# Kernel optimization log

Measured on AMD Instinct MI355X. Metric: run time of the kernel, lower is better.

The kernel has to match this reference:

```python
import jax, jax.numpy as jnp
import numpy as np
from jax import lax

NUM_ITERS = 3
EPSILON = 0.5
QUEUE = 32768
NUM_CLUSTER = 1000


def setup_inputs() -> dict:
    key = jax.random.key(0)
    k1, _ = jax.random.split(key)
    memory_logits = jax.random.normal(k1, (QUEUE, NUM_CLUSTER), dtype=jnp.float32)
    learn_k = jnp.ones((1,), dtype=jnp.float32) * 5.0  # init value in torch module
    return {"memory_logits": memory_logits, "learn_k": learn_k}


def reference(memory_logits, learn_k):
    C = memory_logits.shape[1]
    # stabilize then exp, transpose to [C, N]
    ml = memory_logits - jnp.max(memory_logits)
    Q = jnp.exp(ml / EPSILON).T  # [C, N]
    # K: softmax over clusters of w * log(sigmoid(learn_k)); w = n/(C-1)
    w = (jnp.arange(C, dtype=Q.dtype) / (C - 1)).reshape(1, -1)
    K = jax.nn.softmax(w * jnp.log(jax.nn.sigmoid(learn_k)), axis=1)  # [1, C]
    Kcol = K.reshape(-1, 1)  # [C, 1] for row-wise scaling of Q
    B = Q.shape[1]
    # sort rows by descending row-sum
    order = jnp.argsort(-jnp.sum(Q, axis=1))
    Q = Q[order]
    Q = Q / jnp.sum(Q)

    def body(Q, _):
        Q = Q / jnp.sum(Q, axis=1, keepdims=True)   # row normalize
        Q = Q * Kcol                                 # (Q.t() * K).t()
        Q = jnp.clip(Q, 1e-16, None)
        Q = Q / jnp.sum(Q, axis=0, keepdims=True)   # col normalize
        Q = Q / B
        return Q, None

    Q, _ = lax.scan(body, Q, None, length=NUM_ITERS)
    Q = Q * B
    reorder = jnp.argsort(order)
    Q = Q[reorder]
    return Q.T  # [N, C]
```

## Files before the change

kernel.cpp:

```cpp
#include <hip/hip_runtime.h>
#include <math.h>

#define NQ 32768
#define NC 1000
#define NC4 250

__device__ __forceinline__ float wredsum(float v) {
#pragma unroll
    for (int off = 32; off > 0; off >>= 1) v += __shfl_xor(v, off, 64);
    return v;
}

__global__ __launch_bounds__(256) void k_colsum_exp(const float* __restrict__ in,
                                                    float* __restrict__ S) {
    __shared__ float sacc[NC];
    for (int i = threadIdx.x; i < NC; i += 256) sacc[i] = 0.f;
    __syncthreads();
    const int lane = threadIdx.x & 63;
    const int nw = (gridDim.x * 256) >> 6;
    const int wave = (blockIdx.x * 256 + threadIdx.x) >> 6;
    float acc[16];
#pragma unroll
    for (int i = 0; i < 16; ++i) acc[i] = 0.f;
    for (int row = wave; row < NQ; row += nw) {
        const float4* rp = reinterpret_cast<const float4*>(in + (size_t)row * NC);
#pragma unroll
        for (int k = 0; k < 4; ++k) {
            int c4 = k * 64 + lane;
            if (c4 < NC4) {
                float4 a = rp[c4];
                acc[4 * k + 0] += __expf(2.0f * a.x);
                acc[4 * k + 1] += __expf(2.0f * a.y);
                acc[4 * k + 2] += __expf(2.0f * a.z);
                acc[4 * k + 3] += __expf(2.0f * a.w);
            }
        }
    }
#pragma unroll
    for (int k = 0; k < 4; ++k) {
        int c4 = k * 64 + lane;
        if (c4 < NC4) {
            atomicAdd(&sacc[4 * c4 + 0], acc[4 * k + 0]);
            atomicAdd(&sacc[4 * c4 + 1], acc[4 * k + 1]);
            atomicAdd(&sacc[4 * c4 + 2], acc[4 * k + 2]);
            atomicAdd(&sacc[4 * c4 + 3], acc[4 * k + 3]);
        }
    }
    __syncthreads();
    for (int i = threadIdx.x; i < NC; i += 256) atomicAdd(&S[i], sacc[i]);
}

__global__ __launch_bounds__(1024) void k_rank(const float* __restrict__ S,
                                               const float* __restrict__ learn_k,
                                               float* __restrict__ Ksc,
                                               float* __restrict__ R) {
    __shared__ float sS[NC];
    __shared__ float sred[16];
    const int tid = threadIdx.x;
    for (int i = tid; i < NC; i += 1024) sS[i] = S[i];
    __syncthreads();
    const float L = -log1pf(expf(-learn_k[0]));
    float part = 0.f;
    for (int i = tid; i < NC; i += 1024)
        part += expf(((float)i * (1.0f / 999.0f)) * L);
    part = wredsum(part);
    if ((tid & 63) == 0) sred[tid >> 6] = part;
    __syncthreads();
    if (tid == 0) {
        float s = 0.f;
        for (int i = 0; i < 16; ++i) s += sred[i];
        sred[0] = s;
    }
    __syncthreads();
    const float denom = sred[0];
    for (int c = tid; c < NC; c += 1024) {
        float sc = sS[c];
        int p = 0;
        for (int j = 0; j < NC; ++j) {
            float sj = sS[j];
            p += (sj > sc) || (sj == sc && j < c);
        }
        float ks = expf(((float)p * (1.0f / 999.0f)) * L) / denom;
        Ksc[c] = ks;
        R[c] = ks / sc;
    }
}

__global__ __launch_bounds__(256) void k_prepR(const float* __restrict__ Ksc,
                                               const float* __restrict__ S,
                                               float* __restrict__ R) {
    int i = blockIdx.x * blockDim.x + threadIdx.x;
    if (i < NC) R[i] = Ksc[i] / S[i];
}

template <bool EXPIN, bool ACC>
__global__ __launch_bounds__(256) void k_iter(const float* __restrict__ in,
                                              float* __restrict__ out,
                                              const float* __restrict__ R,
                                              float* __restrict__ Snext) {
    __shared__ float sacc[NC];
    if (ACC) {
        for (int i = threadIdx.x; i < NC; i += 256) sacc[i] = 0.f;
        __syncthreads();
    }
    const int lane = threadIdx.x & 63;
    const int nw = (gridDim.x * 256) >> 6;
    const int wave = (blockIdx.x * 256 + threadIdx.x) >> 6;

    float4 rf[4];
    const float4* R4 = reinterpret_cast<const float4*>(R);
#pragma unroll
    for (int k = 0; k < 4; ++k) {
        int c4 = k * 64 + lane;
        rf[k] = (c4 < NC4) ? R4[c4] : make_float4(0.f, 0.f, 0.f, 0.f);
    }
    float acc[16];
#pragma unroll
    for (int i = 0; i < 16; ++i) acc[i] = 0.f;

    float4 nxt[4];
#pragma unroll
    for (int k = 0; k < 4; ++k) nxt[k] = make_float4(0.f, 0.f, 0.f, 0.f);

    int row = wave;
    if (row < NQ) {
        const float4* rp = reinterpret_cast<const float4*>(in + (size_t)row * NC);
#pragma unroll
        for (int k = 0; k < 4; ++k) {
            int c4 = k * 64 + lane;
            if (c4 < NC4) nxt[k] = rp[c4];
        }
    }
    while (row < NQ) {
        float4 cur[4];
#pragma unroll
        for (int k = 0; k < 4; ++k) cur[k] = nxt[k];
        const int nrow = row + nw;
        if (nrow < NQ) {
            const float4* rp = reinterpret_cast<const float4*>(in + (size_t)nrow * NC);
#pragma unroll
            for (int k = 0; k < 4; ++k) {
                int c4 = k * 64 + lane;
                if (c4 < NC4) nxt[k] = rp[c4];
            }
        }
        float t = 0.f;
#pragma unroll
        for (int k = 0; k < 4; ++k) {
            int c4 = k * 64 + lane;
            if (c4 < NC4) {
                float vx = cur[k].x, vy = cur[k].y, vz = cur[k].z, vw = cur[k].w;
                if (EXPIN) {
                    vx = __expf(2.0f * vx); vy = __expf(2.0f * vy);
                    vz = __expf(2.0f * vz); vw = __expf(2.0f * vw);
                }
                vx = fmaxf(vx * rf[k].x, 1e-16f);
                vy = fmaxf(vy * rf[k].y, 1e-16f);
                vz = fmaxf(vz * rf[k].z, 1e-16f);
                vw = fmaxf(vw * rf[k].w, 1e-16f);
                cur[k] = make_float4(vx, vy, vz, vw);
                t += (vx + vy) + (vz + vw);
            }
        }
        t = wredsum(t);
        const float invt = 1.0f / t;
        float4* op = reinterpret_cast<float4*>(out + (size_t)row * NC);
#pragma unroll
        for (int k = 0; k < 4; ++k) {
            int c4 = k * 64 + lane;
            if (c4 < NC4) {
                float wx = cur[k].x * invt, wy = cur[k].y * invt;
                float wz = cur[k].z * invt, ww = cur[k].w * invt;
                op[c4] = make_float4(wx, wy, wz, ww);
                if (ACC) {
                    acc[4 * k + 0] += wx; acc[4 * k + 1] += wy;
                    acc[4 * k + 2] += wz; acc[4 * k + 3] += ww;
                }
            }
        }
        row = nrow;
    }
    if (ACC) {
#pragma unroll
        for (int k = 0; k < 4; ++k) {
            int c4 = k * 64 + lane;
            if (c4 < NC4) {
                atomicAdd(&sacc[4 * c4 + 0], acc[4 * k + 0]);
                atomicAdd(&sacc[4 * c4 + 1], acc[4 * k + 1]);
                atomicAdd(&sacc[4 * c4 + 2], acc[4 * k + 2]);
                atomicAdd(&sacc[4 * c4 + 3], acc[4 * k + 3]);
            }
        }
        __syncthreads();
        for (int i = threadIdx.x; i < NC; i += 256) atomicAdd(&Snext[i], sacc[i]);
    }
}

extern "C" void kernel_launch(void* const* d_in, const int* in_sizes, int n_in,
                              void* d_out, int out_size, void* d_ws, size_t ws_size,
                              hipStream_t stream) {
    const float* logits = (const float*)d_in[0];
    const float* learn_k = (const float*)d_in[1];
    float* out = (float*)d_out;
    float* ws = (float*)d_ws;
    float* S0 = ws;
    float* S1 = ws + 1024;
    float* S2 = ws + 2048;
    float* Ksc = ws + 3072;
    float* R = ws + 4096;

    hipMemsetAsync(ws, 0, 3072 * sizeof(float), stream);

    const int blocks = 1024;
    k_colsum_exp<<<blocks, 256, 0, stream>>>(logits, S0);
    k_rank<<<1, 1024, 0, stream>>>(S0, learn_k, Ksc, R);
    k_iter<true, true><<<blocks, 256, 0, stream>>>(logits, out, R, S1);
    k_prepR<<<4, 256, 0, stream>>>(Ksc, S1, R);
    k_iter<false, true><<<blocks, 256, 0, stream>>>(out, out, R, S2);
    k_prepR<<<4, 256, 0, stream>>>(Ksc, S2, R);
    k_iter<false, false><<<blocks, 256, 0, stream>>>(out, out, R, nullptr);
}
```

Before: 424.4 us.

## Recompute exp from input each pass using per-column scale vectors instead of intermediates

Result: slower. 451.1 us (+6.3%).

```diff
diff --git a/kernel.cpp b/kernel.cpp
--- a/kernel.cpp
+++ b/kernel.cpp
@@ -4,6 +4,8 @@
 #define NQ 32768
 #define NC 1000
 #define NC4 250
+#define NB 1024
+#define PSTRIDE 1024
 
 __device__ __forceinline__ float wredsum(float v) {
 #pragma unroll
@@ -11,112 +13,33 @@
     return v;
 }
 
-__global__ __launch_bounds__(256) void k_colsum_exp(const float* __restrict__ in,
-                                                    float* __restrict__ S) {
+template <int MODE>
+__global__ __launch_bounds__(256) void k_pass(const float* __restrict__ in,
+                                              const float* __restrict__ svec,
+                                              float* __restrict__ outp) {
     __shared__ float sacc[NC];
-    for (int i = threadIdx.x; i < NC; i += 256) sacc[i] = 0.f;
-    __syncthreads();
+    if (MODE < 2) {
+        for (int i = threadIdx.x; i < NC; i += 256) sacc[i] = 0.f;
+        __syncthreads();
+    }
     const int lane = threadIdx.x & 63;
     const int nw = (gridDim.x * 256) >> 6;
     const int wave = (blockIdx.x * 256 + threadIdx.x) >> 6;
+
+    float4 sf[4];
+    if (MODE >= 1) {
+        const float4* S4 = reinterpret_cast<const float4*>(svec);
+#pragma unroll
+        for (int k = 0; k < 4; ++k) {
+            int c4 = k * 64 + lane;
+            sf[k] = (c4 < NC4) ? S4[c4] : make_float4(0.f, 0.f, 0.f, 0.f);
+        }
+    }
     float acc[16];
-#pragma unroll
-    for (int i = 0; i < 16; ++i) acc[i] = 0.f;
-    for (int row = wave; row < NQ; row += nw) {
-        const float4* rp = reinterpret_cast<const float4*>(in + (size_t)row * NC);
-#pragma unroll
-        for (int k = 0; k < 4; ++k) {
-            int c4 = k * 64 + lane;
-            if (c4 < NC4) {
-                float4 a = rp[c4];
-                acc[4 * k + 0] += __expf(2.0f * a.x);
-                acc[4 * k + 1] += __expf(2.0f * a.y);
-                acc[4 * k + 2] += __expf(2.0f * a.z);
-                acc[4 * k + 3] += __expf(2.0f * a.w);
-            }
-        }
-    }
-#pragma unroll
-    for (int k = 0; k < 4; ++k) {
-        int c4 = k * 64 + lane;
-        if (c4 < NC4) {
-            atomicAdd(&sacc[4 * c4 + 0], acc[4 * k + 0]);
-            atomicAdd(&sacc[4 * c4 + 1], acc[4 * k + 1]);
-            atomicAdd(&sacc[4 * c4 + 2], acc[4 * k + 2]);
-            atomicAdd(&sacc[4 * c4 + 3], acc[4 * k + 3]);
-        }
-    }
-    __syncthreads();
-    for (int i = threadIdx.x; i < NC; i += 256) atomicAdd(&S[i], sacc[i]);
-}
-
-__global__ __launch_bounds__(1024) void k_rank(const float* __restrict__ S,
-                                               const float* __restrict__ learn_k,
-                                               float* __restrict__ Ksc,
-                                               float* __restrict__ R) {
-    __shared__ float sS[NC];
-    __shared__ float sred[16];
-    const int tid = threadIdx.x;
-    for (int i = tid; i < NC; i += 1024) sS[i] = S[i];
-    __syncthreads();
-    const float L = -log1pf(expf(-learn_k[0]));
-    float part = 0.f;
-    for (int i = tid; i < NC; i += 1024)
-        part += expf(((float)i * (1.0f / 999.0f)) * L);
-    part = wredsum(part);
-    if ((tid & 63) == 0) sred[tid >> 6] = part;
-    __syncthreads();
-    if (tid == 0) {
-        float s = 0.f;
-        for (int i = 0; i < 16; ++i) s += sred[i];
-        sred[0] = s;
-    }
-    __syncthreads();
-    const float denom = sred[0];
-    for (int c = tid; c < NC; c += 1024) {
-        float sc = sS[c];
-        int p = 0;
-        for (int j = 0; j < NC; ++j) {
-            float sj = sS[j];
-            p += (sj > sc) || (sj == sc && j < c);
-        }
-        float ks = expf(((float)p * (1.0f / 999.0f)) * L) / denom;
-        Ksc[c] = ks;
-        R[c] = ks / sc;
-    }
-}
-
-__global__ __launch_bounds__(256) void k_prepR(const float* __restrict__ Ksc,
-                                               const float* __restrict__ S,
-                                               float* __restrict__ R) {
-    int i = blockIdx.x * blockDim.x + threadIdx.x;
-    if (i < NC) R[i] = Ksc[i] / S[i];
-}
-
-template <bool EXPIN, bool ACC>
-__global__ __launch_bounds__(256) void k_iter(const float* __restrict__ in,
-                                              float* __restrict__ out,
-                                              const float* __restrict__ R,
-                                              float* __restrict__ Snext) {
-    __shared__ float sacc[NC];
-    if (ACC) {
-        for (int i = threadIdx.x; i < NC; i += 256) sacc[i] = 0.f;
-        __syncthreads();
-    }
-    const int lane = threadIdx.x & 63;
-    const int nw = (gridDim.x * 256) >> 6;
-    const int wave = (blockIdx.x * 256 + threadIdx.x) >> 6;
-
-    float4 rf[4];
-    const float4* R4 = reinterpret_cast<const float4*>(R);
-#pragma unroll
-    for (int k = 0; k < 4; ++k) {
-        int c4 = k * 64 + lane;
-        rf[k] = (c4 < NC4) ? R4[c4] : make_float4(0.f, 0.f, 0.f, 0.f);
-    }
-    float acc[16];
-#pragma unroll
-    for (int i = 0; i < 16; ++i) acc[i] = 0.f;
+    if (MODE < 2) {
+#pragma unroll
+        for (int i = 0; i < 16; ++i) acc[i] = 0.f;
+    }
 
     float4 nxt[4];
 #pragma unroll
@@ -144,43 +67,52 @@
                 if (c4 < NC4) nxt[k] = rp[c4];
             }
         }
-        float t = 0.f;
-#pragma unroll
-        for (int k = 0; k < 4; ++k) {
-            int c4 = k * 64 + lane;
-            if (c4 < NC4) {
-                float vx = cur[k].x, vy = cur[k].y, vz = cur[k].z, vw = cur[k].w;
-                if (EXPIN) {
-                    vx = __expf(2.0f * vx); vy = __expf(2.0f * vy);
-                    vz = __expf(2.0f * vz); vw = __expf(2.0f * vw);
+        float4 e[4];
+#pragma unroll
+        for (int k = 0; k < 4; ++k) {
+            e[k].x = __expf(2.f * cur[k].x);
+            e[k].y = __expf(2.f * cur[k].y);
+            e[k].z = __expf(2.f * cur[k].z);
+            e[k].w = __expf(2.f * cur[k].w);
+        }
+        if (MODE == 0) {
+#pragma unroll
+            for (int k = 0; k < 4; ++k) {
+                acc[4 * k + 0] += e[k].x; acc[4 * k + 1] += e[k].y;
+                acc[4 * k + 2] += e[k].z; acc[4 * k + 3] += e[k].w;
+            }
+        } else {
+            float t = 0.f;
+#pragma unroll
+            for (int k = 0; k < 4; ++k) {
+                t += e[k].x * sf[k].x + e[k].y * sf[k].y
+                   + e[k].z * sf[k].z + e[k].w * sf[k].w;
+            }
+            t = wredsum(t);
+            const float r = 1.0f / t;
+            if (MODE == 1) {
+#pragma unroll
+                for (int k = 0; k < 4; ++k) {
+                    acc[4 * k + 0] += e[k].x * r; acc[4 * k + 1] += e[k].y * r;
+                    acc[4 * k + 2] += e[k].z * r; acc[4 * k + 3] += e[k].w * r;
                 }
-                vx = fmaxf(vx * rf[k].x, 1e-16f);
-                vy = fmaxf(vy * rf[k].y, 1e-16f);
-                vz = fmaxf(vz * rf[k].z, 1e-16f);
-                vw = fmaxf(vw * rf[k].w, 1e-16f);
-                cur[k] = make_float4(vx, vy, vz, vw);
-                t += (vx + vy) + (vz + vw);
-            }
-        }
-        t = wredsum(t);
-        const float invt = 1.0f / t;
-        float4* op = reinterpret_cast<float4*>(out + (size_t)row * NC);
-#pragma unroll
-        for (int k = 0; k < 4; ++k) {
-            int c4 = k * 64 + lane;
-            if (c4 < NC4) {
-                float wx = cur[k].x * invt, wy = cur[k].y * invt;
-                float wz = cur[k].z * invt, ww = cur[k].w * invt;
-                op[c4] = make_float4(wx, wy, wz, ww);
-                if (ACC) {
-                    acc[4 * k + 0] += wx; acc[4 * k + 1] += wy;
-                    acc[4 * k + 2] += wz; acc[4 * k + 3] += ww;
+            } else {
+                float4* op = reinterpret_cast<float4*>(outp + (size_t)row * NC);
+#pragma unroll
+                for (int k = 0; k < 4; ++k) {
+                    int c4 = k * 64 + lane;
+                    if (c4 < NC4) {
+                        op[c4] = make_float4(e[k].x * sf[k].x * r,
+                                             e[k].y * sf[k].y * r,
+                                             e[k].z * sf[k].z * r,
+                                             e[k].w * sf[k].w * r);
+                    }
                 }
             }
         }
         row = nrow;
     }
-    if (ACC) {
+    if (MODE < 2) {
 #pragma unroll
         for (int k = 0; k < 4; ++k) {
             int c4 = k * 64 + lane;
@@ -192,31 +124,88 @@
             }
         }
         __syncthreads();
-        for (int i = threadIdx.x; i < NC; i += 256) atomicAdd(&Snext[i], sacc[i]);
-    }
+        float* prow = outp + (size_t)blockIdx.x * PSTRIDE;
+        for (int i = threadIdx.x; i < NC; i += 256) prow[i] = sacc[i];
+    }
+}
+
+__global__ __launch_bounds__(128) void k_reduceG(const float* __restrict__ part,
+                                                 float* __restrict__ G) {
+    const int c = (blockIdx.x & 7) * 128 + threadIdx.x;
+    const int p0 = (blockIdx.x >> 3) * 256;
+    if (c < NC) {
+        float sum = 0.f;
+        for (int p = p0; p < p0 + 256; p += 4) {
+            sum += part[(size_t)p * PSTRIDE + c]
+                 + part[(size_t)(p + 1) * PSTRIDE + c]
+                 + part[(size_t)(p + 2) * PSTRIDE + c]
+                 + part[(size_t)(p + 3) * PSTRIDE + c];
+        }
+        atomicAdd(&G[c], sum);
+    }
+}
+
+__global__ __launch_bounds__(128) void k_rank(const float* __restrict__ G,
+                                              const float* __restrict__ learn_k,
+                                              float* __restrict__ Ksc,
+                                              float* __restrict__ svec) {
+    __shared__ float sS[NC];
+    __shared__ float sred[2];
+    for (int i = threadIdx.x; i < NC; i += 128) sS[i] = G[i];
+    const float L = -log1pf(expf(-learn_k[0]));
+    float part = 0.f;
+    for (int i = threadIdx.x; i < NC; i += 128)
+        part += expf((float)i * (1.0f / 999.0f) * L);
+    part = wredsum(part);
+    if ((threadIdx.x & 63) == 0) sred[threadIdx.x >> 6] = part;
+    __syncthreads();
+    const float denom = sred[0] + sred[1];
+    const int c = blockIdx.x * 128 + threadIdx.x;
+    if (c < NC) {
+        const float sc = sS[c];
+        int p = 0;
+#pragma unroll 4
+        for (int j = 0; j < NC; ++j) {
+            float sj = sS[j];
+            p += (sj > sc) || (sj == sc && j < c);
+        }
+        const float ks = expf((float)p * (1.0f / 999.0f) * L) / denom;
+        Ksc[c] = ks;
+        svec[c] = ks / sc;
+    }
+}
+
+__global__ __launch_bounds__(256) void k_prepS(const float* __restrict__ Ksc,
+                                               const float* __restrict__ G,
+                                               float* __restrict__ svec) {
+    const int i = blockIdx.x * 256 + threadIdx.x;
+    if (i < NC) svec[i] = Ksc[i] / G[i];
 }
 
 extern "C" void kernel_launch(void* const* d_in, const int* in_sizes, int n_in,
                               void* d_out, int out_size, void* d_ws, size_t ws_size,
                               hipStream_t stream) {
-    const float* logits = (const float*)d_in[0];
-    const float* learn_k = (const float*)d_in[1];
+    const float* A = (const float*)d_in[0];
+    const float* lk = (const float*)d_in[1];
     float* out = (float*)d_out;
     float* ws = (float*)d_ws;
-    float* S0 = ws;
-    float* S1 = ws + 1024;
-    float* S2 = ws + 2048;
+    float* G0 = ws;
+    float* G1 = ws + 1024;
+    float* G2 = ws + 2048;
     float* Ksc = ws + 3072;
-    float* R = ws + 4096;
+    float* sv = ws + 4096;
+    float* part = ws + 8192;
 
     hipMemsetAsync(ws, 0, 3072 * sizeof(float), stream);
 
-    const int blocks = 1024;
-    k_colsum_exp<<<blocks, 256, 0, stream>>>(logits, S0);
-    k_rank<<<1, 1024, 0, stream>>>(S0, learn_k, Ksc, R);
-    k_iter<true, true><<<blocks, 256, 0, stream>>>(logits, out, R, S1);
-    k_prepR<<<4, 256, 0, stream>>>(Ksc, S1, R);
-    k_iter<false, true><<<blocks, 256, 0, stream>>>(out, out, R, S2);
-    k_prepR<<<4, 256, 0, stream>>>(Ksc, S2, R);
-    k_iter<false, false><<<blocks, 256, 0, stream>>>(out, out, R, nullptr);
-}
+    k_pass<0><<<NB, 256, 0, stream>>>(A, nullptr, part);
+    k_reduceG<<<32, 128, 0, stream>>>(part, G0);
+    k_rank<<<8, 128, 0, stream>>>(G0, lk, Ksc, sv);
+    k_pass<1><<<NB, 256, 0, stream>>>(A, sv, part);
+    k_reduceG<<<32, 128, 0, stream>>>(part, G1);
+    k_prepS<<<4, 256, 0, stream>>>(Ksc, G1, sv);
+    k_pass<1><<<NB, 256, 0, stream>>>(A, sv, part);
+    k_reduceG<<<32, 128, 0, stream>>>(part, G2);
+    k_prepS<<<4, 256, 0, stream>>>(Ksc, G2, sv);
+    k_pass<2><<<NB, 256, 0, stream>>>(A, sv, out);
+}
```
